# Optimization experiments

Measured on AMD Instinct MI355X. Metric: run time of the kernel, lower is better.

The kernel has to match this reference:

```python
import jax, jax.numpy as jnp
import numpy as np

D_MODEL = 512
D_INNER = 2 * D_MODEL      # 1024
DT_RANK = D_MODEL // 16    # 32
D_STATE = 16
D_CONV = 4
NB_LAYERS = 3
BATCH = 64
SEQ = 201
CITY = 200
EPS = 1e-5


def setup_inputs() -> dict:
    key = jax.random.key(0)
    ks = jax.random.split(key, 12)
    def rn(k, shape, scale=0.02):
        return jax.random.normal(k, shape, jnp.float32) * scale
    A_init = jnp.tile(jnp.arange(1, D_STATE + 1, dtype=jnp.float32)[None, None, :],
                      (NB_LAYERS, D_INNER, 1))
    return {
        "x": jax.random.uniform(ks[0], (BATCH, SEQ, 2), jnp.float32),
        "city_count": CITY,
        "embed_W": rn(ks[1], (D_MODEL, 2), 0.5),
        "embed_b": jnp.zeros((D_MODEL,), jnp.float32),
        "norm_w": jnp.ones((NB_LAYERS, D_MODEL), jnp.float32),
        "norm_b": jnp.zeros((NB_LAYERS, D_MODEL), jnp.float32),
        "in_W": rn(ks[2], (NB_LAYERS, 2 * D_INNER, D_MODEL)),
        "conv_w": rn(ks[3], (NB_LAYERS, D_INNER, D_CONV), 0.1),
        "conv_b": jnp.zeros((NB_LAYERS, D_INNER), jnp.float32),
        "xproj_W": rn(ks[4], (NB_LAYERS, DT_RANK + 2 * D_STATE, D_INNER)),
        "dtproj_W": rn(ks[5], (NB_LAYERS, D_INNER, DT_RANK), 0.1),
        "dtproj_b": rn(ks[6], (NB_LAYERS, D_INNER), 0.5),
        "A_log": jnp.log(A_init),
        "Dskip": jnp.ones((NB_LAYERS, D_INNER), jnp.float32),
        "out_W": rn(ks[7], (NB_LAYERS, D_MODEL, D_INNER)),
        "normf_w": jnp.ones((D_MODEL,), jnp.float32),
        "normf_b": jnp.zeros((D_MODEL,), jnp.float32),
        "head_W": rn(ks[8], (CITY, D_MODEL)),
    }


def _silu(v):
    return v * jax.nn.sigmoid(v)


def _layernorm(v, w, b):
    v = v.astype(jnp.float32)
    mu = v.mean(-1, keepdims=True)
    var = ((v - mu) ** 2).mean(-1, keepdims=True)
    return (v - mu) * jax.lax.rsqrt(var + EPS) * w + b


def _rmsnorm(v, w, b):
    v = v.astype(jnp.float32)
    ms = (v * v).mean(-1, keepdims=True)
    return v * jax.lax.rsqrt(ms + EPS) * w + b


def _mamba_mixer(h, in_W, cw, cb, xp_W, dt_W, dt_b, A_log, Dv, o_W):
    B, L, _ = h.shape
    xz = jnp.einsum('bld,ed->ble', h, in_W)              # (B,L,2*di)
    xc, z = jnp.split(xz, 2, axis=-1)
    # causal depthwise conv over time
    xt = xc.transpose(0, 2, 1)                           # (B,di,L)
    xt = jax.lax.conv_general_dilated(
        xt, cw[:, None, :], (1,), [(D_CONV - 1, 0)],
        dimension_numbers=('NCH', 'OIH', 'NCH'),
        feature_group_count=D_INNER)
    u = _silu((xt + cb[None, :, None]).transpose(0, 2, 1))   # (B,L,di)
    x_dbl = jnp.einsum('bld,ed->ble', u, xp_W)
    dt_r = x_dbl[..., :DT_RANK]
    Bm = x_dbl[..., DT_RANK:DT_RANK + D_STATE]
    Cm = x_dbl[..., DT_RANK + D_STATE:]
    dt = jax.nn.softplus(jnp.einsum('blr,dr->bld', dt_r, dt_W) + dt_b)
    A = -jnp.exp(A_log)                                  # (di,n)

    def step(hst, ins):
        dt_t, B_t, C_t, u_t = ins                        # (B,di),(B,n),(B,n),(B,di)
        dA = jnp.exp(dt_t[..., None] * A)                # (B,di,n)
        hst = dA * hst + (dt_t * u_t)[..., None] * B_t[:, None, :]
        y = jnp.einsum('bdn,bn->bd', hst, C_t)
        return hst, y

    h0 = jnp.zeros((B, D_INNER, D_STATE), h.dtype)
    _, ys = jax.lax.scan(step, h0, (dt.transpose(1, 0, 2), Bm.transpose(1, 0, 2),
                                    Cm.transpose(1, 0, 2), u.transpose(1, 0, 2)))
    y = ys.transpose(1, 0, 2) + Dv * u
    y = y * _silu(z)
    return jnp.einsum('bld,ed->ble', y, o_W)


def reference(x, city_count, embed_W, embed_b, norm_w, norm_b, in_W, conv_w, conv_b,
              xproj_W, dtproj_W, dtproj_b, A_log, Dskip, out_W, normf_w, normf_b, head_W):
    h = jnp.einsum('blc,dc->bld', x, embed_W) + embed_b
    residual = None
    for i in range(NB_LAYERS):
        residual = h if residual is None else h + residual   # residual in fp32
        hn = _layernorm(residual, norm_w[i], norm_b[i])
        h = _mamba_mixer(hn, in_W[i], conv_w[i], conv_b[i], xproj_W[i],
                         dtproj_W[i], dtproj_b[i], A_log[i], Dskip[i], out_W[i])
    residual = h + residual
    xf = _rmsnorm(residual, normf_w, normf_b)                # final fused RMSNorm
    logits = jnp.einsum('bld,cd->blc', xf, head_W)           # output head -> city logits
    return logits
```

## Files before the change

### kernel.cpp

```cpp
#include <hip/hip_runtime.h>
#include <hip/hip_fp16.h>
#include <math.h>

#define D_MODEL 512
#define D_INNER 1024
#define DT_RANK 32
#define D_STATE 16
#define D_CONV 4
#define NB_LAYERS 3
#define BATCH 64
#define SEQ 201
#define CITY 200
#define M_ROWS (BATCH * SEQ)
#define M_PAD 12928
#define EPS 1e-5f
#define NCH 8
#define CL 26

typedef __attribute__((ext_vector_type(8))) short short8;
typedef __attribute__((ext_vector_type(8))) unsigned short ushort8;
typedef __attribute__((ext_vector_type(4))) float f32x4;

__device__ __forceinline__ float sigmoidf_(float x) { return 1.f / (1.f + __expf(-x)); }

__device__ __forceinline__ unsigned short f2b(float f) {
  union { float f; unsigned int u; } v; v.f = f;
  unsigned int r = (v.u + 0x7fff + ((v.u >> 16) & 1)) >> 16;
  return (unsigned short)r;
}
__device__ __forceinline__ float b2f(unsigned short h) {
  union { unsigned int u; float f; } v; v.u = ((unsigned int)h) << 16; return v.f;
}
__device__ __forceinline__ unsigned short f2h(float f) {
  __half h = __float2half(f); return *(unsigned short*)&h;
}
__device__ __forceinline__ float h2f(unsigned short u) {
  __half h = *(__half*)&u; return __half2float(h);
}

__device__ __forceinline__ void gload_lds16(const void* g, void* l) {
  __builtin_amdgcn_global_load_lds(
      (const __attribute__((address_space(1))) void*)g,
      (__attribute__((address_space(3))) void*)l, 16, 0, 0);
}

__global__ __launch_bounds__(256) void k_f2b(const float* __restrict__ in,
                                             unsigned short* __restrict__ out,
                                             int n, int n_total) {
  int i = blockIdx.x * 256 + threadIdx.x;
  if (i < n) out[i] = f2b(in[i]);
  else if (i < n_total) out[i] = 0;
}

__global__ __launch_bounds__(256) void k_padW(const float* __restrict__ W,
                                              unsigned short* __restrict__ out,
                                              int rows, int incols, int outcols) {
  int i = blockIdx.x * 256 + threadIdx.x;
  if (i >= rows * outcols) return;
  int n = i / outcols, k = i - n * outcols;
  out[i] = (k < incols) ? f2b(W[(size_t)n * incols + k]) : 0;
}

__global__ __launch_bounds__(256) void k_padR(const float* __restrict__ W,
                                              unsigned short* __restrict__ out,
                                              int nl, int inrows, int outrows, int cols) {
  int i = blockIdx.x * 256 + threadIdx.x;
  if (i >= nl * outrows * cols) return;
  int c = i % cols;
  int r = (i / cols) % outrows;
  int L = i / (cols * outrows);
  out[i] = (r < inrows) ? f2b(W[((size_t)L * inrows + r) * cols + c]) : 0;
}

__global__ __launch_bounds__(256) void k_convT(const float* __restrict__ cw,
                                               float* __restrict__ cwT) {
  int i = blockIdx.x * 256 + threadIdx.x;
  if (i >= NB_LAYERS * D_CONV * D_INNER) return;
  int d = i & (D_INNER - 1);
  int k = (i >> 10) & 3;
  int L = i >> 12;
  cwT[i] = cw[((size_t)L * D_INNER + d) * D_CONV + k];
}

__global__ __launch_bounds__(256) void k_embed(const float* __restrict__ x,
                                               const float* __restrict__ W,
                                               const float* __restrict__ b,
                                               float* __restrict__ h) {
  int idx = blockIdx.x * 256 + threadIdx.x;
  if (idx >= M_ROWS * D_MODEL) return;
  int d = idx & (D_MODEL - 1);
  int m = idx >> 9;
  float x0 = x[m * 2 + 0], x1 = x[m * 2 + 1];
  h[idx] = fmaf(x0, W[d * 2 + 0], fmaf(x1, W[d * 2 + 1], b[d]));
}

__global__ __launch_bounds__(256) void k_resid_norm(const float* __restrict__ h,
                                                    float* __restrict__ resid,
                                                    float* __restrict__ out,
                                                    unsigned short* __restrict__ out_b,
                                                    const float* __restrict__ w,
                                                    const float* __restrict__ b,
                                                    int addRes, int mode) {
  int row = blockIdx.x * 4 + (threadIdx.x >> 6);
  int lane = threadIdx.x & 63;
  if (row >= M_ROWS) return;
  const float* hp = h + (size_t)row * D_MODEL;
  float* rp = resid + (size_t)row * D_MODEL;
  float v[8];
#pragma unroll
  for (int j = 0; j < 8; ++j) {
    float t = hp[j * 64 + lane];
    if (addRes) t += rp[j * 64 + lane];
    v[j] = t;
    rp[j * 64 + lane] = t;
  }
  float mu = 0.f, rstd;
  if (mode == 0) {
    float s = 0.f;
#pragma unroll
    for (int j = 0; j < 8; ++j) s += v[j];
#pragma unroll
    for (int o = 1; o < 64; o <<= 1) s += __shfl_xor(s, o);
    mu = s * (1.f / D_MODEL);
    float vs = 0.f;
#pragma unroll
    for (int j = 0; j < 8; ++j) { float d0 = v[j] - mu; vs += d0 * d0; }
#pragma unroll
    for (int o = 1; o < 64; o <<= 1) vs += __shfl_xor(vs, o);
    rstd = rsqrtf(vs * (1.f / D_MODEL) + EPS);
  } else {
    float s = 0.f;
#pragma unroll
    for (int j = 0; j < 8; ++j) s += v[j] * v[j];
#pragma unroll
    for (int o = 1; o < 64; o <<= 1) s += __shfl_xor(s, o);
    rstd = rsqrtf(s * (1.f / D_MODEL) + EPS);
  }
#pragma unroll
  for (int j = 0; j < 8; ++j) {
    int c = j * 64 + lane;
    float o = (v[j] - mu) * rstd * w[c] + b[c];
    if (out) out[(size_t)row * D_MODEL + c] = o;
    if (out_b) out_b[(size_t)row * D_MODEL + c] = f2b(o);
  }
}

template <int BOUT, int ACT>
__global__ __launch_bounds__(256) void k_gemm_mfma(const unsigned short* __restrict__ A,
                                                   const unsigned short* __restrict__ B,
                                                   const float* __restrict__ bias,
                                                   void* __restrict__ Cv, int ldc,
                                                   int M, int Nout, int K) {
  __shared__ unsigned short lA[128 * 64];
  __shared__ unsigned short lB[128 * 64];
  int tid = threadIdx.x;
  int wave = tid >> 6, lane = tid & 63;
  int nx = gridDim.x;
  int nwg = nx * gridDim.y;
  int bid = blockIdx.y * nx + blockIdx.x;
  int q = nwg >> 3, rr = nwg & 7;
  int xcd = bid & 7, idx = bid >> 3;
  int swz = (xcd < rr ? xcd * (q + 1) : rr * (q + 1) + (xcd - rr) * q) + idx;
  int bm = (swz / nx) * 128, bn = (swz % nx) * 128;
  int wm = (wave >> 1) * 64, wn = (wave & 1) * 64;
  f32x4 acc[4][4] = {};

  for (int k0 = 0; k0 < K; k0 += 64) {
#pragma unroll
    for (int i = 0; i < 4; ++i) {
      int e = (i * 256 + tid) * 8;
      int r = e >> 6, c = e & 63;
      int csrc = c ^ ((r & 7) << 3);
      gload_lds16(A + (size_t)(bm + r) * K + k0 + csrc, &lA[e]);
      gload_lds16(B + (size_t)(bn + r) * K + k0 + csrc, &lB[e]);
    }
    __syncthreads();
#pragma unroll
    for (int ks = 0; ks < 2; ++ks) {
      int koff = ks * 32 + (lane >> 4) * 8;
      short8 a[4], b[4];
#pragma unroll
      for (int i = 0; i < 4; ++i) {
        int row = wm + i * 16 + (lane & 15);
        a[i] = *(const short8*)&lA[row * 64 + (koff ^ ((row & 7) << 3))];
      }
#pragma unroll
      for (int j = 0; j < 4; ++j) {
        int row = wn + j * 16 + (lane & 15);
        b[j] = *(const short8*)&lB[row * 64 + (koff ^ ((row & 7) << 3))];
      }
#pragma unroll
      for (int i = 0; i < 4; ++i)
#pragma unroll
        for (int j = 0; j < 4; ++j)
          acc[i][j] = __builtin_amdgcn_mfma_f32_16x16x32_bf16(a[i], b[j], acc[i][j], 0, 0, 0);
    }
    __syncthreads();
  }
#pragma unroll
  for (int i = 0; i < 4; ++i) {
    int row0 = bm + wm + i * 16 + (lane >> 4) * 4;
#pragma unroll
    for (int j = 0; j < 4; ++j) {
      int col = bn + wn + j * 16 + (lane & 15);
#pragma unroll
      for (int r = 0; r < 4; ++r) {
        int m = row0 + r;
        if (m < M && col < Nout) {
          float v = acc[i][j][r];
          if (ACT) { v += bias[col]; v = (v > 20.f) ? v : __logf(1.f + __expf(v)); }
          if (BOUT == 1) ((unsigned short*)Cv)[(size_t)m * ldc + col] = f2b(v);
          else if (BOUT == 2) ((unsigned short*)Cv)[(size_t)m * ldc + col] = f2h(v);
          else ((float*)Cv)[(size_t)m * ldc + col] = v;
        }
      }
    }
  }
}

__global__ __launch_bounds__(256) void k_conv_silu(const unsigned short* __restrict__ xz,
                                                   const float* __restrict__ cwT,
                                                   const float* __restrict__ cb,
                                                   unsigned short* __restrict__ ub) {
  int i = blockIdx.x * 256 + threadIdx.x;
  if (i >= M_ROWS * 128) return;
  int dg = (i & 127) << 3;
  int m = i >> 7;
  int l = m % SEQ;
  float y[8];
  float4 cb0 = *(const float4*)&cb[dg];
  float4 cb1 = *(const float4*)&cb[dg + 4];
  y[0] = cb0.x; y[1] = cb0.y; y[2] = cb0.z; y[3] = cb0.w;
  y[4] = cb1.x; y[5] = cb1.y; y[6] = cb1.z; y[7] = cb1.w;
#pragma unroll
  for (int k = 0; k < D_CONV; ++k) {
    int ls = l - (D_CONV - 1) + k;
    if (ls >= 0) {
      ushort8 xv = *(const ushort8*)&xz[(size_t)(m - (D_CONV - 1) + k) * 2048 + dg];
      float4 w0 = *(const float4*)&cwT[k * D_INNER + dg];
      float4 w1 = *(const float4*)&cwT[k * D_INNER + dg + 4];
      y[0] = fmaf(w0.x, b2f(xv[0]), y[0]);
      y[1] = fmaf(w0.y, b2f(xv[1]), y[1]);
      y[2] = fmaf(w0.z, b2f(xv[2]), y[2]);
      y[3] = fmaf(w0.w, b2f(xv[3]), y[3]);
      y[4] = fmaf(w1.x, b2f(xv[4]), y[4]);
      y[5] = fmaf(w1.y, b2f(xv[5]), y[5]);
      y[6] = fmaf(w1.z, b2f(xv[6]), y[6]);
      y[7] = fmaf(w1.w, b2f(xv[7]), y[7]);
    }
  }
  ushort8 o;
#pragma unroll
  for (int j = 0; j < 8; ++j) { float v = y[j]; v = v * sigmoidf_(v); o[j] = f2b(v); }
  *(ushort8*)&ub[(size_t)m * D_INNER + dg] = o;
}

__global__ __launch_bounds__(256) void k_scan_p1(const unsigned short* __restrict__ dt,
                                                 const unsigned short* __restrict__ ub,
                                                 const unsigned short* __restrict__ xdb,
                                                 const float* __restrict__ A_log,
                                                 unsigned short* __restrict__ L,
                                                 float* __restrict__ dtsum) {
  int tid = threadIdx.x;
  int b = blockIdx.x >> 3, c = blockIdx.x & 7;
  int d = blockIdx.y * 256 + tid;
  int t0 = c * CL, t1 = t0 + CL < SEQ ? t0 + CL : SEQ;
  float Areg[D_STATE], hst[D_STATE];
#pragma unroll
  for (int n = 0; n < D_STATE; ++n) {
    Areg[n] = -__expf(A_log[d * D_STATE + n]);
    hst[n] = 0.f;
  }
  float ds = 0.f;
  size_t row0 = (size_t)b * SEQ;
  for (int t = t0; t < t1; ++t) {
    size_t m = row0 + t;
    float dtv = h2f(dt[m * D_INNER + d]);
    float uv = b2f(ub[m * D_INNER + d]);
    const unsigned short* xp = xdb + m * 64 + 32;
    ushort8 b0 = *(const ushort8*)&xp[0];
    ushort8 b1 = *(const ushort8*)&xp[8];
    float du = dtv * uv;
    ds += dtv;
#pragma unroll
    for (int j = 0; j < 8; ++j)
      hst[j] = fmaf(__expf(dtv * Areg[j]), hst[j], du * b2f(b0[j]));
#pragma unroll
    for (int j = 0; j < 8; ++j)
      hst[8 + j] = fmaf(__expf(dtv * Areg[8 + j]), hst[8 + j], du * b2f(b1[j]));
  }
  size_t base = ((size_t)(b * NCH + c) * D_INNER + d) * D_STATE;
  ushort8 o0, o1;
#pragma unroll
  for (int j = 0; j < 8; ++j) { o0[j] = f2b(hst[j]); o1[j] = f2b(hst[8 + j]); }
  *(ushort8*)&L[base] = o0;
  *(ushort8*)&L[base + 8] = o1;
  dtsum[(size_t)(b * NCH + c) * D_INNER + d] = ds;
}

__global__ __launch_bounds__(256) void k_scan_fix(const float* __restrict__ A_log,
                                                  const float* __restrict__ dtsum,
                                                  unsigned short* __restrict__ L) {
  int tid = threadIdx.x;
  int b = blockIdx.x;
  int d = blockIdx.y * 256 + tid;
  float Areg[D_STATE], h[D_STATE];
#pragma unroll
  for (int n = 0; n < D_STATE; ++n) {
    Areg[n] = -__expf(A_log[d * D_STATE + n]);
    h[n] = 0.f;
  }
  for (int c = 0; c < NCH; ++c) {
    size_t base = ((size_t)(b * NCH + c) * D_INNER + d) * D_STATE;
    ushort8 l0 = *(const ushort8*)&L[base];
    ushort8 l1 = *(const ushort8*)&L[base + 8];
    float ds = dtsum[(size_t)(b * NCH + c) * D_INNER + d];
    ushort8 o0, o1;
#pragma unroll
    for (int j = 0; j < 8; ++j) { o0[j] = f2b(h[j]); o1[j] = f2b(h[8 + j]); }
    *(ushort8*)&L[base] = o0;
    *(ushort8*)&L[base + 8] = o1;
#pragma unroll
    for (int j = 0; j < 8; ++j)
      h[j] = fmaf(__expf(Areg[j] * ds), h[j], b2f(l0[j]));
#pragma unroll
    for (int j = 0; j < 8; ++j)
      h[8 + j] = fmaf(__expf(Areg[8 + j] * ds), h[8 + j], b2f(l1[j]));
  }
}

__global__ __launch_bounds__(256) void k_scan_p2(const unsigned short* __restrict__ dt,
                                                 const unsigned short* __restrict__ xz,
                                                 const unsigned short* __restrict__ ub,
                                                 const unsigned short* __restrict__ xdb,
                                                 const float* __restrict__ A_log,
                                                 const float* __restrict__ Dv,
                                                 const unsigned short* __restrict__ L,
                                                 unsigned short* __restrict__ yb) {
  int tid = threadIdx.x;
  int b = blockIdx.x >> 3, c = blockIdx.x & 7;
  int d = blockIdx.y * 256 + tid;
  int t0 = c * CL, t1 = t0 + CL < SEQ ? t0 + CL : SEQ;
  float Areg[D_STATE], hst[D_STATE];
  size_t base = ((size_t)(b * NCH + c) * D_INNER + d) * D_STATE;
  ushort8 l0 = *(const ushort8*)&L[base];
  ushort8 l1 = *(const ushort8*)&L[base + 8];
#pragma unroll
  for (int n = 0; n < D_STATE; ++n) Areg[n] = -__expf(A_log[d * D_STATE + n]);
#pragma unroll
  for (int j = 0; j < 8; ++j) { hst[j] = b2f(l0[j]); hst[8 + j] = b2f(l1[j]); }
  float Dd = Dv[d];
  size_t row0 = (size_t)b * SEQ;
  for (int t = t0; t < t1; ++t) {
    size_t m = row0 + t;
    float dtv = h2f(dt[m * D_INNER + d]);
    float uv = b2f(ub[m * D_INNER + d]);
    float zv = b2f(xz[m * 2048 + 1024 + d]);
    const unsigned short* xp = xdb + m * 64 + 32;
    ushort8 b0 = *(const ushort8*)&xp[0];
    ushort8 b1 = *(const ushort8*)&xp[8];
    ushort8 c0 = *(const ushort8*)&xp[16];
    ushort8 c1 = *(const ushort8*)&xp[24];
    float du = dtv * uv;
    float y0 = 0.f, y1 = 0.f, y2 = 0.f, y3 = 0.f;
#pragma unroll
    for (int j = 0; j < 8; ++j) {
      hst[j] = fmaf(__expf(dtv * Areg[j]), hst[j], du * b2f(b0[j]));
      float& yq = (j < 4) ? y0 : y1;
      yq = fmaf(hst[j], b2f(c0[j]), yq);
    }
#pragma unroll
    for (int j = 0; j < 8; ++j) {
      hst[8 + j] = fmaf(__expf(dtv * Areg[8 + j]), hst[8 + j], du * b2f(b1[j]));
      float& yq = (j < 4) ? y2 : y3;
      yq = fmaf(hst[8 + j], b2f(c1[j]), yq);
    }
    float y = (y0 + y1) + (y2 + y3);
    y = fmaf(Dd, uv, y);
    y = y * (zv * sigmoidf_(zv));
    yb[m * D_INNER + d] = f2b(y);
  }
}

extern "C" void kernel_launch(void* const* d_in, const int* in_sizes, int n_in,
                              void* d_out, int out_size, void* d_ws, size_t ws_size,
                              hipStream_t stream) {
  const float* x        = (const float*)d_in[0];
  const float* embed_W  = (const float*)d_in[2];
  const float* embed_b  = (const float*)d_in[3];
  const float* norm_w   = (const float*)d_in[4];
  const float* norm_b   = (const float*)d_in[5];
  const float* in_W     = (const float*)d_in[6];
  const float* conv_w   = (const float*)d_in[7];
  const float* conv_b   = (const float*)d_in[8];
  const float* xproj_W  = (const float*)d_in[9];
  const float* dtproj_W = (const float*)d_in[10];
  const float* dtproj_b = (const float*)d_in[11];
  const float* A_log    = (const float*)d_in[12];
  const float* Dskip    = (const float*)d_in[13];
  const float* out_W    = (const float*)d_in[14];
  const float* normf_w  = (const float*)d_in[15];
  const float* normf_b  = (const float*)d_in[16];
  const float* head_W   = (const float*)d_in[17];
  float* out = (float*)d_out;

  size_t bf16_elems = (size_t)M_ROWS * 2048 + (size_t)M_PAD * 2048 + (size_t)M_PAD * 64 +
                      (size_t)NB_LAYERS * (2048 * 512 + 512 * 1024 + 128 * 1024 + 1024 * 64) +
                      256 * 512;
  size_t need = (size_t)M_ROWS * 1024 * 4 + (size_t)M_ROWS * 1024 * 2 + bf16_elems * 2 +
                (size_t)NB_LAYERS * D_CONV * D_INNER * 4;
  if (ws_size < need) return;

  float* ws = (float*)d_ws;
  float* buf_res  = ws;
  float* buf_h    = buf_res  + (size_t)M_ROWS * 512;
  unsigned short* buf_dt   = (unsigned short*)(buf_h + (size_t)M_ROWS * 512);
  unsigned short* buf_xz   = buf_dt + (size_t)M_ROWS * 1024;
  unsigned short* buf_ub   = buf_xz + (size_t)M_ROWS * 2048;
  unsigned short* buf_yb   = buf_ub + (size_t)M_PAD * 1024;
  unsigned short* buf_hnb  = buf_yb;
  unsigned short* buf_xdb  = buf_yb + (size_t)M_PAD * 1024;
  unsigned short* buf_wib  = buf_xdb + (size_t)M_PAD * 64;
  unsigned short* buf_wob  = buf_wib + (size_t)NB_LAYERS * 2048 * 512;
  unsigned short* buf_wxb  = buf_wob + (size_t)NB_LAYERS * 512 * 1024;
  unsigned short* buf_wdtb = buf_wxb + (size_t)NB_LAYERS * 128 * 1024;
  unsigned short* buf_whb  = buf_wdtb + (size_t)NB_LAYERS * 1024 * 64;
  float* buf_cwT = (float*)(buf_whb + (size_t)256 * 512);

  unsigned short* buf_L = (unsigned short*)buf_h;
  float* buf_dts = (float*)(buf_L + (size_t)BATCH * NCH * D_INNER * D_STATE);

  dim3 blk(256);

  k_f2b<<<(NB_LAYERS * 2048 * 512 + 255) / 256, blk, 0, stream>>>(
      in_W, buf_wib, NB_LAYERS * 2048 * 512, NB_LAYERS * 2048 * 512);
  k_f2b<<<(NB_LAYERS * 512 * 1024 + 255) / 256, blk, 0, stream>>>(
      out_W, buf_wob, NB_LAYERS * 512 * 1024, NB_LAYERS * 512 * 1024);
  k_padR<<<(NB_LAYERS * 128 * 1024 + 255) / 256, blk, 0, stream>>>(
      xproj_W, buf_wxb, NB_LAYERS, 64, 128, 1024);
  k_padW<<<(NB_LAYERS * 1024 * 64 + 255) / 256, blk, 0, stream>>>(
      dtproj_W, buf_wdtb, NB_LAYERS * 1024, DT_RANK, 64);
  k_f2b<<<(256 * 512 + 255) / 256, blk, 0, stream>>>(head_W, buf_whb, CITY * 512, 256 * 512);
  k_convT<<<(NB_LAYERS * D_CONV * D_INNER + 255) / 256, blk, 0, stream>>>(conv_w, buf_cwT);

  k_embed<<<(M_ROWS * D_MODEL + 255) / 256, blk, 0, stream>>>(x, embed_W, embed_b, buf_h);

  for (int i = 0; i < NB_LAYERS; ++i) {
    k_resid_norm<<<(M_ROWS + 3) / 4, blk, 0, stream>>>(
        buf_h, buf_res, nullptr, buf_hnb, norm_w + i * D_MODEL, norm_b + i * D_MODEL,
        i > 0 ? 1 : 0, 0);

    k_gemm_mfma<1, 0><<<dim3(2048 / 128, M_PAD / 128), blk, 0, stream>>>(
        buf_hnb, buf_wib + (size_t)i * 2048 * 512, nullptr, buf_xz, 2048, M_ROWS, 2048, 512);

    k_conv_silu<<<(M_ROWS * 128 + 255) / 256, blk, 0, stream>>>(
        buf_xz, buf_cwT + (size_t)i * D_CONV * D_INNER, conv_b + (size_t)i * D_INNER, buf_ub);

    k_gemm_mfma<1, 0><<<dim3(1, M_PAD / 128), blk, 0, stream>>>(
        buf_ub, buf_wxb + (size_t)i * 128 * 1024, nullptr, buf_xdb, 64, M_ROWS, 64, 1024);

    k_gemm_mfma<2, 1><<<dim3(1024 / 128, M_PAD / 128), blk, 0, stream>>>(
        buf_xdb, buf_wdtb + (size_t)i * 1024 * 64, dtproj_b + (size_t)i * D_INNER,
        buf_dt, 1024, M_ROWS, 1024, 64);

    const float* Ai = A_log + (size_t)i * D_INNER * D_STATE;
    k_scan_p1<<<dim3(BATCH * NCH, D_INNER / 256), blk, 0, stream>>>(
        buf_dt, buf_ub, buf_xdb, Ai, buf_L, buf_dts);
    k_scan_fix<<<dim3(BATCH, D_INNER / 256), blk, 0, stream>>>(Ai, buf_dts, buf_L);
    k_scan_p2<<<dim3(BATCH * NCH, D_INNER / 256), blk, 0, stream>>>(
        buf_dt, buf_xz, buf_ub, buf_xdb, Ai, Dskip + (size_t)i * D_INNER, buf_L, buf_yb);

    k_gemm_mfma<0, 0><<<dim3(512 / 128, M_PAD / 128), blk, 0, stream>>>(
        buf_yb, buf_wob + (size_t)i * 512 * 1024, nullptr, buf_h, 512, M_ROWS, 512, 1024);
  }

  k_resid_norm<<<(M_ROWS + 3) / 4, blk, 0, stream>>>(
      buf_h, buf_res, nullptr, buf_hnb, normf_w, normf_b, 1, 1);

  k_gemm_mfma<0, 0><<<dim3(256 / 128, M_PAD / 128), blk, 0, stream>>>(
      buf_hnb, buf_whb, nullptr, out, CITY, M_ROWS, CITY, 512);
}
```

Measured before the change: 814.2 us.

## Fuse dt projection and softplus into both scan passes, drop dt GEMM

Removes the separate dt_proj GEMM and its fp16 dt buffer. Each scan thread now holds its 32 dt_proj weights in registers and computes the dot product with the low-rank xdb row plus bias and softplus inline, in both scan passes. This avoids writing and re-reading a 12928x1024 fp16 tensor twice per layer. In exchange the dot product is computed twice, once per pass, and adds register pressure in the scan kernels.

```diff
diff --git a/kernel.cpp b/kernel.cpp
--- a/kernel.cpp
+++ b/kernel.cpp
@@ -31,12 +31,6 @@
 __device__ __forceinline__ float b2f(unsigned short h) {
   union { unsigned int u; float f; } v; v.u = ((unsigned int)h) << 16; return v.f;
 }
-__device__ __forceinline__ unsigned short f2h(float f) {
-  __half h = __float2half(f); return *(unsigned short*)&h;
-}
-__device__ __forceinline__ float h2f(unsigned short u) {
-  __half h = *(__half*)&u; return __half2float(h);
-}
 
 __device__ __forceinline__ void gload_lds16(const void* g, void* l) {
   __builtin_amdgcn_global_load_lds(
@@ -50,15 +44,6 @@
   int i = blockIdx.x * 256 + threadIdx.x;
   if (i < n) out[i] = f2b(in[i]);
   else if (i < n_total) out[i] = 0;
-}
-
-__global__ __launch_bounds__(256) void k_padW(const float* __restrict__ W,
-                                              unsigned short* __restrict__ out,
-                                              int rows, int incols, int outcols) {
-  int i = blockIdx.x * 256 + threadIdx.x;
-  if (i >= rows * outcols) return;
-  int n = i / outcols, k = i - n * outcols;
-  out[i] = (k < incols) ? f2b(W[(size_t)n * incols + k]) : 0;
 }
 
 __global__ __launch_bounds__(256) void k_padR(const float* __restrict__ W,
@@ -145,10 +130,9 @@
   }
 }
 
-template <int BOUT, int ACT>
+template <int BOUT>
 __global__ __launch_bounds__(256) void k_gemm_mfma(const unsigned short* __restrict__ A,
                                                    const unsigned short* __restrict__ B,
-                                                   const float* __restrict__ bias,
                                                    void* __restrict__ Cv, int ldc,
                                                    int M, int Nout, int K) {
   __shared__ unsigned short lA[128 * 64];
@@ -208,9 +192,7 @@
         int m = row0 + r;
         if (m < M && col < Nout) {
           float v = acc[i][j][r];
-          if (ACT) { v += bias[col]; v = (v > 20.f) ? v : __logf(1.f + __expf(v)); }
           if (BOUT == 1) ((unsigned short*)Cv)[(size_t)m * ldc + col] = f2b(v);
-          else if (BOUT == 2) ((unsigned short*)Cv)[(size_t)m * ldc + col] = f2h(v);
           else ((float*)Cv)[(size_t)m * ldc + col] = v;
         }
       }
@@ -255,9 +237,28 @@
   *(ushort8*)&ub[(size_t)m * D_INNER + dg] = o;
 }
 
-__global__ __launch_bounds__(256) void k_scan_p1(const unsigned short* __restrict__ dt,
-                                                 const unsigned short* __restrict__ ub,
+__device__ __forceinline__ float dt_eval(const unsigned short* __restrict__ xq,
+                                         const float* __restrict__ Wd, float bias) {
+  ushort8 r0 = *(const ushort8*)&xq[0];
+  ushort8 r1 = *(const ushort8*)&xq[8];
+  ushort8 r2 = *(const ushort8*)&xq[16];
+  ushort8 r3 = *(const ushort8*)&xq[24];
+  float a0 = 0.f, a1 = 0.f, a2 = 0.f, a3 = 0.f;
+#pragma unroll
+  for (int j = 0; j < 8; ++j) {
+    a0 = fmaf(b2f(r0[j]), Wd[j], a0);
+    a1 = fmaf(b2f(r1[j]), Wd[8 + j], a1);
+    a2 = fmaf(b2f(r2[j]), Wd[16 + j], a2);
+    a3 = fmaf(b2f(r3[j]), Wd[24 + j], a3);
+  }
+  float dot = ((a0 + a1) + (a2 + a3)) + bias;
+  return (dot > 20.f) ? dot : __logf(1.f + __expf(dot));
+}
+
+__global__ __launch_bounds__(256) void k_scan_p1(const unsigned short* __restrict__ ub,
                                                  const unsigned short* __restrict__ xdb,
+                                                 const float* __restrict__ dtW,
+                                                 const float* __restrict__ dtb,
                                                  const float* __restrict__ A_log,
                                                  unsigned short* __restrict__ L,
                                                  float* __restrict__ dtsum) {
@@ -265,6 +266,13 @@
   int b = blockIdx.x >> 3, c = blockIdx.x & 7;
   int d = blockIdx.y * 256 + tid;
   int t0 = c * CL, t1 = t0 + CL < SEQ ? t0 + CL : SEQ;
+  float Wd[DT_RANK];
+#pragma unroll
+  for (int r = 0; r < DT_RANK; r += 4) {
+    float4 w4 = *(const float4*)&dtW[(size_t)d * DT_RANK + r];
+    Wd[r] = w4.x; Wd[r + 1] = w4.y; Wd[r + 2] = w4.z; Wd[r + 3] = w4.w;
+  }
+  float bias = dtb[d];
   float Areg[D_STATE], hst[D_STATE];
 #pragma unroll
   for (int n = 0; n < D_STATE; ++n) {
@@ -275,11 +283,11 @@
   size_t row0 = (size_t)b * SEQ;
   for (int t = t0; t < t1; ++t) {
     size_t m = row0 + t;
-    float dtv = h2f(dt[m * D_INNER + d]);
+    const unsigned short* xq = xdb + m * 64;
+    float dtv = dt_eval(xq, Wd, bias);
     float uv = b2f(ub[m * D_INNER + d]);
-    const unsigned short* xp = xdb + m * 64 + 32;
-    ushort8 b0 = *(const ushort8*)&xp[0];
-    ushort8 b1 = *(const ushort8*)&xp[8];
+    ushort8 b0 = *(const ushort8*)&xq[32];
+    ushort8 b1 = *(const ushort8*)&xq[40];
     float du = dtv * uv;
     ds += dtv;
 #pragma unroll
@@ -329,10 +337,11 @@
   }
 }
 
-__global__ __launch_bounds__(256) void k_scan_p2(const unsigned short* __restrict__ dt,
-                                                 const unsigned short* __restrict__ xz,
+__global__ __launch_bounds__(256) void k_scan_p2(const unsigned short* __restrict__ xz,
                                                  const unsigned short* __restrict__ ub,
                                                  const unsigned short* __restrict__ xdb,
+                                                 const float* __restrict__ dtW,
+                                                 const float* __restrict__ dtb,
                                                  const float* __restrict__ A_log,
                                                  const float* __restrict__ Dv,
                                                  const unsigned short* __restrict__ L,
@@ -341,6 +350,13 @@
   int b = blockIdx.x >> 3, c = blockIdx.x & 7;
   int d = blockIdx.y * 256 + tid;
   int t0 = c * CL, t1 = t0 + CL < SEQ ? t0 + CL : SEQ;
+  float Wd[DT_RANK];
+#pragma unroll
+  for (int r = 0; r < DT_RANK; r += 4) {
+    float4 w4 = *(const float4*)&dtW[(size_t)d * DT_RANK + r];
+    Wd[r] = w4.x; Wd[r + 1] = w4.y; Wd[r + 2] = w4.z; Wd[r + 3] = w4.w;
+  }
+  float bias = dtb[d];
   float Areg[D_STATE], hst[D_STATE];
   size_t base = ((size_t)(b * NCH + c) * D_INNER + d) * D_STATE;
   ushort8 l0 = *(const ushort8*)&L[base];
@@ -353,14 +369,14 @@
   size_t row0 = (size_t)b * SEQ;
   for (int t = t0; t < t1; ++t) {
     size_t m = row0 + t;
-    float dtv = h2f(dt[m * D_INNER + d]);
+    const unsigned short* xq = xdb + m * 64;
+    float dtv = dt_eval(xq, Wd, bias);
     float uv = b2f(ub[m * D_INNER + d]);
     float zv = b2f(xz[m * 2048 + 1024 + d]);
-    const unsigned short* xp = xdb + m * 64 + 32;
-    ushort8 b0 = *(const ushort8*)&xp[0];
-    ushort8 b1 = *(const ushort8*)&xp[8];
-    ushort8 c0 = *(const ushort8*)&xp[16];
-    ushort8 c1 = *(const ushort8*)&xp[24];
+    ushort8 b0 = *(const ushort8*)&xq[32];
+    ushort8 b1 = *(const ushort8*)&xq[40];
+    ushort8 c0 = *(const ushort8*)&xq[48];
+    ushort8 c1 = *(const ushort8*)&xq[56];
     float du = dtv * uv;
     float y0 = 0.f, y1 = 0.f, y2 = 0.f, y3 = 0.f;
 #pragma unroll
@@ -405,17 +421,16 @@
   float* out = (float*)d_out;
 
   size_t bf16_elems = (size_t)M_ROWS * 2048 + (size_t)M_PAD * 2048 + (size_t)M_PAD * 64 +
-                      (size_t)NB_LAYERS * (2048 * 512 + 512 * 1024 + 128 * 1024 + 1024 * 64) +
+                      (size_t)NB_LAYERS * (2048 * 512 + 512 * 1024 + 128 * 1024) +
                       256 * 512;
-  size_t need = (size_t)M_ROWS * 1024 * 4 + (size_t)M_ROWS * 1024 * 2 + bf16_elems * 2 +
+  size_t need = (size_t)M_ROWS * 1024 * 4 + bf16_elems * 2 +
                 (size_t)NB_LAYERS * D_CONV * D_INNER * 4;
   if (ws_size < need) return;
 
   float* ws = (float*)d_ws;
   float* buf_res  = ws;
   float* buf_h    = buf_res  + (size_t)M_ROWS * 512;
-  unsigned short* buf_dt   = (unsigned short*)(buf_h + (size_t)M_ROWS * 512);
-  unsigned short* buf_xz   = buf_dt + (size_t)M_ROWS * 1024;
+  unsigned short* buf_xz   = (unsigned short*)(buf_h + (size_t)M_ROWS * 512);
   unsigned short* buf_ub   = buf_xz + (size_t)M_ROWS * 2048;
   unsigned short* buf_yb   = buf_ub + (size_t)M_PAD * 1024;
   unsigned short* buf_hnb  = buf_yb;
@@ -423,8 +438,7 @@
   unsigned short* buf_wib  = buf_xdb + (size_t)M_PAD * 64;
   unsigned short* buf_wob  = buf_wib + (size_t)NB_LAYERS * 2048 * 512;
   unsigned short* buf_wxb  = buf_wob + (size_t)NB_LAYERS * 512 * 1024;
-  unsigned short* buf_wdtb = buf_wxb + (size_t)NB_LAYERS * 128 * 1024;
-  unsigned short* buf_whb  = buf_wdtb + (size_t)NB_LAYERS * 1024 * 64;
+  unsigned short* buf_whb  = buf_wxb + (size_t)NB_LAYERS * 128 * 1024;
   float* buf_cwT = (float*)(buf_whb + (size_t)256 * 512);
 
   unsigned short* buf_L = (unsigned short*)buf_h;
@@ -438,8 +452,6 @@
       out_W, buf_wob, NB_LAYERS * 512 * 1024, NB_LAYERS * 512 * 1024);
   k_padR<<<(NB_LAYERS * 128 * 1024 + 255) / 256, blk, 0, stream>>>(
       xproj_W, buf_wxb, NB_LAYERS, 64, 128, 1024);
-  k_padW<<<(NB_LAYERS * 1024 * 64 + 255) / 256, blk, 0, stream>>>(
-      dtproj_W, buf_wdtb, NB_LAYERS * 1024, DT_RANK, 64);
   k_f2b<<<(256 * 512 + 255) / 256, blk, 0, stream>>>(head_W, buf_whb, CITY * 512, 256 * 512);
   k_convT<<<(NB_LAYERS * D_CONV * D_INNER + 255) / 256, blk, 0, stream>>>(conv_w, buf_cwT);
 
@@ -450,33 +462,31 @@
         buf_h, buf_res, nullptr, buf_hnb, norm_w + i * D_MODEL, norm_b + i * D_MODEL,
         i > 0 ? 1 : 0, 0);
 
-    k_gemm_mfma<1, 0><<<dim3(2048 / 128, M_PAD / 128), blk, 0, stream>>>(
-        buf_hnb, buf_wib + (size_t)i * 2048 * 512, nullptr, buf_xz, 2048, M_ROWS, 2048, 512);
+    k_gemm_mfma<1><<<dim3(2048 / 128, M_PAD / 128), blk, 0, stream>>>(
+        buf_hnb, buf_wib + (size_t)i * 2048 * 512, buf_xz, 2048, M_ROWS, 2048, 512);
 
     k_conv_silu<<<(M_ROWS * 128 + 255) / 256, blk, 0, stream>>>(
         buf_xz, buf_cwT + (size_t)i * D_CONV * D_INNER, conv_b + (size_t)i * D_INNER, buf_ub);
 
-    k_gemm_mfma<1, 0><<<dim3(1, M_PAD / 128), blk, 0, stream>>>(
-        buf_ub, buf_wxb + (size_t)i * 128 * 1024, nullptr, buf_xdb, 64, M_ROWS, 64, 1024);
-
-    k_gemm_mfma<2, 1><<<dim3(1024 / 128, M_PAD / 128), blk, 0, stream>>>(
-        buf_xdb, buf_wdtb + (size_t)i * 1024 * 64, dtproj_b + (size_t)i * D_INNER,
-        buf_dt, 1024, M_ROWS, 1024, 64);
-
-    const float* Ai = A_log + (size_t)i * D_INNER * D_STATE;
+    k_gemm_mfma<1><<<dim3(1, M_PAD / 128), blk, 0, stream>>>(
+        buf_ub, buf_wxb + (size_t)i * 128 * 1024, buf_xdb, 64, M_ROWS, 64, 1024);
+
+    const float* Ai  = A_log + (size_t)i * D_INNER * D_STATE;
+    const float* Wdt = dtproj_W + (size_t)i * D_INNER * DT_RANK;
+    const float* bdt = dtproj_b + (size_t)i * D_INNER;
     k_scan_p1<<<dim3(BATCH * NCH, D_INNER / 256), blk, 0, stream>>>(
-        buf_dt, buf_ub, buf_xdb, Ai, buf_L, buf_dts);
+        buf_ub, buf_xdb, Wdt, bdt, Ai, buf_L, buf_dts);
     k_scan_fix<<<dim3(BATCH, D_INNER / 256), blk, 0, stream>>>(Ai, buf_dts, buf_L);
     k_scan_p2<<<dim3(BATCH * NCH, D_INNER / 256), blk, 0, stream>>>(
-        buf_dt, buf_xz, buf_ub, buf_xdb, Ai, Dskip + (size_t)i * D_INNER, buf_L, buf_yb);
-
-    k_gemm_mfma<0, 0><<<dim3(512 / 128, M_PAD / 128), blk, 0, stream>>>(
-        buf_yb, buf_wob + (size_t)i * 512 * 1024, nullptr, buf_h, 512, M_ROWS, 512, 1024);
+        buf_xz, buf_ub, buf_xdb, Wdt, bdt, Ai, Dskip + (size_t)i * D_INNER, buf_L, buf_yb);
+
+    k_gemm_mfma<0><<<dim3(512 / 128, M_PAD / 128), blk, 0, stream>>>(
+        buf_yb, buf_wob + (size_t)i * 512 * 1024, buf_h, 512, M_ROWS, 512, 1024);
   }
 
   k_resid_norm<<<(M_ROWS + 3) / 4, blk, 0, stream>>>(
       buf_h, buf_res, nullptr, buf_hnb, normf_w, normf_b, 1, 1);
 
-  k_gemm_mfma<0, 0><<<dim3(256 / 128, M_PAD / 128), blk, 0, stream>>>(
-      buf_hnb, buf_whb, nullptr, out, CITY, M_ROWS, CITY, 512);
-}
+  k_gemm_mfma<0><<<dim3(256 / 128, M_PAD / 128), blk, 0, stream>>>(
+      buf_hnb, buf_whb, out, CITY, M_ROWS, CITY, 512);
+}
```

Result: no change. 809.7 us (-0.6%).
